# Kernel optimization log

Hardware: AMD Instinct MI355X
Metric: run time of the kernel (lower is better)

The kernel has to match this reference:

```python
import jax, jax.numpy as jnp
from jax import lax
import numpy as np

K_TOP = 100
NMS_THRESH = 0.5
SUBJECT_CATEGORY_ID = 0


def box_cxcywh_to_xyxy(b):
    cx, cy, w, h = b[..., 0], b[..., 1], b[..., 2], b[..., 3]
    return jnp.stack([cx - 0.5 * w, cy - 0.5 * h, cx + 0.5 * w, cy + 0.5 * h], axis=-1)


def _pairwise_iou(boxes):
    # boxes: [K,4] xyxy; uses the +1 pixel convention from the original numpy NMS
    x1, y1, x2, y2 = boxes[:, 0], boxes[:, 1], boxes[:, 2], boxes[:, 3]
    area = (x2 - x1 + 1.0) * (y2 - y1 + 1.0)
    xx1 = jnp.maximum(x1[:, None], x1[None, :])
    yy1 = jnp.maximum(y1[:, None], y1[None, :])
    xx2 = jnp.minimum(x2[:, None], x2[None, :])
    yy2 = jnp.minimum(y2[:, None], y2[None, :])
    w = jnp.maximum(0.0, xx2 - xx1 + 1.0)
    h = jnp.maximum(0.0, yy2 - yy1 + 1.0)
    inter = w * h
    union = area[:, None] + area[None, :] - inter
    return inter / union


def _nms_keep(sub_boxes, obj_boxes, obj_labels, hoi_scores):
    # Greedy grouped pairwise NMS for one image.
    # Grouping key degenerates to object label (subject cat and verb-row are constant).
    K = sub_boxes.shape[0]
    max_scores = hoi_scores.max(axis=-1)
    order = jnp.argsort(-max_scores)
    ovr = _pairwise_iou(sub_boxes) * _pairwise_iou(obj_boxes)  # [K,K]
    same_group = obj_labels[:, None] == obj_labels[None, :]
    ovr = jnp.where(same_group, ovr, 0.0)
    ovr_s = ovr[order][:, order]
    upper = jnp.triu(jnp.ones((K, K), dtype=bool), k=1)
    sup_mat = (ovr_s > NMS_THRESH) & upper  # suppression only of later (lower-score) items

    def body(i, st):
        suppressed, keep = st
        ki = jnp.logical_not(suppressed[i])
        keep = keep.at[i].set(ki)
        suppressed = suppressed | (ki & sup_mat[i])
        return suppressed, keep

    _, keep_sorted = lax.fori_loop(0, K, body, (jnp.zeros(K, bool), jnp.zeros(K, bool)))
    return jnp.zeros(K, bool).at[order].set(keep_sorted)


def setup_inputs() -> dict:
    key = jax.random.key(0)
    k1, k2, k3, k4, k5, k6 = jax.random.split(key, 6)
    B, Q, C, V = 256, 300, 81, 117
    return {
        "pred_obj_logits": jax.random.normal(k1, (B, Q, C), dtype=jnp.float32),
        "pred_verb_logits": jax.random.normal(k2, (B, Q, V), dtype=jnp.float32),
        "pred_sub_boxes": jax.random.uniform(k3, (B, Q, 4), dtype=jnp.float32),
        "pred_obj_boxes": jax.random.uniform(k4, (B, Q, 4), dtype=jnp.float32),
        "correct_mat": (jax.random.uniform(k5, (V, C), dtype=jnp.float32) > 0.3).astype(jnp.float32),
        "target_sizes": jax.random.randint(k6, (B, 2), 200, 640, dtype=jnp.int32),
    }


def reference(pred_obj_logits, pred_verb_logits, pred_sub_boxes, pred_obj_boxes, correct_mat, target_sizes):
    B, Q, C = pred_obj_logits.shape
    V = pred_verb_logits.shape[-1]

    obj_prob = jax.nn.softmax(pred_obj_logits, axis=-1)       # [B,Q,C]  (no_obj=False)
    verb_scores = jax.nn.sigmoid(pred_verb_logits)            # [B,Q,V]

    topk_values, topk_indexes = lax.top_k(obj_prob.reshape(B, Q * C), K_TOP)  # [B,100]
    topk_boxes = topk_indexes // C
    obj_labels = topk_indexes % C

    vs = jnp.take_along_axis(verb_scores, topk_boxes[..., None], axis=1)      # [B,100,V]
    ob = jnp.take_along_axis(pred_obj_boxes, topk_boxes[..., None], axis=1)   # [B,100,4]
    sb = jnp.take_along_axis(pred_sub_boxes, topk_boxes[..., None], axis=1)

    img_h = target_sizes[:, 0].astype(jnp.float32)
    img_w = target_sizes[:, 1].astype(jnp.float32)
    scale_fct = jnp.stack([img_w, img_h, img_w, img_h], axis=1)  # [B,4]
    sub_boxes = box_cxcywh_to_xyxy(sb) * scale_fct[:, None, :]
    obj_boxes = box_cxcywh_to_xyxy(ob) * scale_fct[:, None, :]

    hoi_scores = vs * topk_values[..., None]                    # [B,100,V]
    # masks[b,k,v] = correct_mat[v, obj_labels[b,k]]
    masks = correct_mat.T[obj_labels]                           # [B,100,V]
    hoi_scores = hoi_scores * masks

    keep = jax.vmap(_nms_keep)(sub_boxes, obj_boxes, obj_labels, hoi_scores)  # [B,100] bool
    final_scores = hoi_scores * keep[..., None].astype(hoi_scores.dtype)

    return final_scores, topk_values, obj_labels, sub_boxes, obj_boxes, keep
```

## Files before the change

kernel.cpp:

```cpp
#include <hip/hip_runtime.h>
#include <cmath>

#pragma clang fp contract(off)

#define NT 1024
constexpr int B_ = 256, Q_ = 300, C_ = 81, V_ = 117, K_ = 100;
constexpr int QC_ = Q_ * C_;
constexpr int KV_ = K_ * V_;
constexpr int NB  = 2048;
constexpr int CAP = 1024;

using u32 = unsigned int;
using u64 = unsigned long long;
using u16 = unsigned short;
using u8  = unsigned char;

#define PCUT 0.010f

constexpr int OFF_P16  = 0;
constexpr int OFF_HIST = 48600;
constexpr int OFF_RMAX = OFF_HIST + 8192;
constexpr int OFF_RINV = OFF_RMAX + 1200;
constexpr int OFF_BSUB = OFF_RINV + 1208;
constexpr int OFF_BOBJ = OFF_BSUB + 1600;
constexpr int OFF_SUPR = OFF_BOBJ + 1600;
constexpr int OFF_SELV = OFF_SUPR + 1600;
constexpr int OFF_SELI = OFF_SELV + 400;
constexpr int OFF_MAXB = OFF_SELI + 400;
constexpr int OFF_ORD  = OFF_MAXB + 400;
constexpr int OFF_LAB  = OFF_ORD + 104;
constexpr int OFF_MISC = OFF_LAB + 104;
constexpr int SMEM_SZ  = OFF_MISC + 48;
static_assert(SMEM_SZ <= 65536, "LDS overflow");
static_assert((OFF_BSUB & 15) == 0 && (OFF_BOBJ & 15) == 0, "b128 align");

__device__ __forceinline__ u64 shfl_xor_u64(u64 v, int mask) {
    u32 lo = (u32)v, hi = (u32)(v >> 32);
    lo = (u32)__shfl_xor((int)lo, mask, 64);
    hi = (u32)__shfl_xor((int)hi, mask, 64);
    return ((u64)hi << 32) | lo;
}

template <int CTRL>
__device__ __forceinline__ int dpp_i(int x) {
    return __builtin_amdgcn_update_dpp(0, x, CTRL, 0xF, 0xF, true);
}
__device__ __forceinline__ float bfly16(float x){ return __int_as_float(__builtin_amdgcn_ds_swizzle(__float_as_int(x), 0x401F)); }
__device__ __forceinline__ float bfly8 (float x){ return __int_as_float(dpp_i<0x128>(__float_as_int(x))); }
__device__ __forceinline__ float bfly4 (float x){ return __int_as_float(__builtin_amdgcn_ds_swizzle(__float_as_int(x), 0x101F)); }
__device__ __forceinline__ float bfly2 (float x){ return __int_as_float(dpp_i<0x4E>(__float_as_int(x))); }
__device__ __forceinline__ float bfly1 (float x){ return __int_as_float(dpp_i<0xB1>(__float_as_int(x))); }
__device__ __forceinline__ int ibfly4(int x){ return __builtin_amdgcn_ds_swizzle(x, 0x101F); }
__device__ __forceinline__ int ibfly2(int x){ return dpp_i<0x4E>(x); }
__device__ __forceinline__ int ibfly1(int x){ return dpp_i<0xB1>(x); }

__device__ __forceinline__ float iou4(float4 a, float4 b, float areaSum) {
    float xx1 = fmaxf(a.x, b.x);
    float yy1 = fmaxf(a.y, b.y);
    float xx2 = fminf(a.z, b.z);
    float yy2 = fminf(a.w, b.w);
    float w = fmaxf(0.f, xx2 - xx1 + 1.f);
    float h = fmaxf(0.f, yy2 - yy1 + 1.f);
    float inter = w * h;
    return inter / (areaSum - inter);
}

__global__ __launch_bounds__(NT, 4) void hoi_kernel(
    const float* __restrict__ obj_logits,
    const float* __restrict__ verb_logits,
    const float* __restrict__ sub_boxes_in,
    const float* __restrict__ obj_boxes_in,
    const float* __restrict__ cm,
    const int*   __restrict__ tsizes,
    float* __restrict__ out)
{
    const int b = blockIdx.x;
    const int tid = threadIdx.x;

    __shared__ __align__(16) u8 smem[SMEM_SZ];
    u16*   p16     = (u16*)(smem + OFF_P16);
    float* hs      = (float*)(smem + OFF_P16);
    u32*   hist    = (u32*)(smem + OFF_HIST);
    u64*   cand    = (u64*)(smem + OFF_HIST);
    float* asub    = (float*)(smem + OFF_HIST);
    float* aobj    = (float*)(smem + OFF_HIST + 512);
    float* rowmax  = (float*)(smem + OFF_RMAX);
    float* rinv    = (float*)(smem + OFF_RINV);
    float (*bsub)[4]   = (float(*)[4])(smem + OFF_BSUB);
    float (*bobj)[4]   = (float(*)[4])(smem + OFF_BOBJ);
    u32   (*supcol)[4] = (u32(*)[4])(smem + OFF_SUPR);
    float* sel_val = (float*)(smem + OFF_SELV);
    u32*   sel_idx = (u32*)(smem + OFF_SELI);
    u32*   maxbits = (u32*)(smem + OFF_MAXB);
    u8*    order8  = (u8*)(smem + OFF_ORD);
    u8*    lab8    = (u8*)(smem + OFF_LAB);
    u32*   skeep     = (u32*)(smem + OFF_MISC);
    u32*   keep_bits = (u32*)(smem + OFF_MISC + 16);
    u32*   s_cnt     = (u32*)(smem + OFF_MISC + 32);
    int*   sT        = (int*)(smem + OFF_MISC + 36);
    int*   sW        = (int*)(smem + OFF_MISC + 40);
    u32*   sAcc      = (u32*)(smem + OFF_MISC + 44);
    u32*   swsum   = (u32*)(smem + OFF_BSUB);
    u64*   wred    = (u64*)(smem + OFF_BOBJ);
    u64*   s_prev  = (u64*)(smem + OFF_SUPR);

    const float* lg = obj_logits + (size_t)b * QC_;

    for (int i = tid; i < NB; i += NT) hist[i] = 0;
    if (tid == 0) *s_cnt = 0;
    __syncthreads();

    {
        const int g = tid >> 5, l = tid & 31;
        const bool have2 = (l < C_ - 64);
        float v0[10], v1[10], v2[10];
        #pragma unroll
        for (int s = 0; s < 10; ++s) {
            int r = g + 32 * s;
            const float* row = lg + (size_t)((r < Q_ ? r : Q_ - 1) * C_);
            v0[s] = row[l];
            v1[s] = row[l + 32];
            v2[s] = have2 ? row[l + 64] : -INFINITY;
        }
        float m[10];
        #pragma unroll
        for (int s = 0; s < 10; ++s) m[s] = fmaxf(fmaxf(v0[s], v1[s]), v2[s]);
        #pragma unroll
        for (int s = 0; s < 10; ++s) m[s] = fmaxf(m[s], bfly16(m[s]));
        #pragma unroll
        for (int s = 0; s < 10; ++s) m[s] = fmaxf(m[s], bfly8(m[s]));
        #pragma unroll
        for (int s = 0; s < 10; ++s) m[s] = fmaxf(m[s], bfly4(m[s]));
        #pragma unroll
        for (int s = 0; s < 10; ++s) m[s] = fmaxf(m[s], bfly2(m[s]));
        #pragma unroll
        for (int s = 0; s < 10; ++s) m[s] = fmaxf(m[s], bfly1(m[s]));
        float e0[10], e1[10], e2[10], sm[10];
        #pragma unroll
        for (int s = 0; s < 10; ++s) {
            e0[s] = expf(v0[s] - m[s]);
            e1[s] = expf(v1[s] - m[s]);
            e2[s] = have2 ? expf(v2[s] - m[s]) : 0.f;
            sm[s] = e0[s] + e1[s] + e2[s];
        }
        #pragma unroll
        for (int s = 0; s < 10; ++s) sm[s] += bfly16(sm[s]);
        #pragma unroll
        for (int s = 0; s < 10; ++s) sm[s] += bfly8(sm[s]);
        #pragma unroll
        for (int s = 0; s < 10; ++s) sm[s] += bfly4(sm[s]);
        #pragma unroll
        for (int s = 0; s < 10; ++s) sm[s] += bfly2(sm[s]);
        #pragma unroll
        for (int s = 0; s < 10; ++s) sm[s] += bfly1(sm[s]);
        #pragma unroll
        for (int s = 0; s < 10; ++s) {
            int r = g + 32 * s;
            if (r < Q_) {
                float ri = 1.f / sm[s];
                float p0 = e0[s] * ri, p1 = e1[s] * ri;
                u32 x0 = __float_as_uint(p0), x1 = __float_as_uint(p1);
                p16[r * C_ + l]      = (u16)(x0 >> 16);
                p16[r * C_ + l + 32] = (u16)(x1 >> 16);
                if (p0 >= PCUT) atomicAdd(&hist[x0 >> 21], 1u);
                if (p1 >= PCUT) atomicAdd(&hist[x1 >> 21], 1u);
                if (have2) {
                    float p2 = e2[s] * ri;
                    u32 x2 = __float_as_uint(p2);
                    p16[r * C_ + l + 64] = (u16)(x2 >> 16);
                    if (p2 >= PCUT) atomicAdd(&hist[x2 >> 21], 1u);
                }
                if (l == 0) { rowmax[r] = m[s]; rinv[r] = ri; }
            }
        }
    }
    __syncthreads();

    u32 my_c, my_suf;
    {
        int t = tid;
        my_c = hist[2 * t] + hist[2 * t + 1];
        my_suf = my_c;
        #pragma unroll
        for (int off = 1; off < 64; off <<= 1) {
            u32 o = (u32)__shfl_down((int)my_suf, off, 64);
            my_suf += ((tid & 63) + off < 64) ? o : 0;
        }
        if ((tid & 63) == 0) swsum[tid >> 6] = my_suf;
    }
    __syncthreads();
    if (tid < 16) {
        u32 sufW = swsum[tid];
        #pragma unroll
        for (int off = 1; off < 16; off <<= 1) {
            u32 o = (u32)__shfl_down((int)sufW, off, 64);
            sufW += (tid + off < 16) ? o : 0;
        }
        u32 nxt = (u32)__shfl_down((int)sufW, 1, 64);
        if (tid == 15) nxt = 0;
        if (sufW >= (u32)K_ && nxt < (u32)K_) { *sW = tid; *sAcc = nxt; }
    }
    __syncthreads();
    if ((tid >> 6) == *sW) {
        u32 above = *sAcc + (my_suf - my_c);
        if (above < (u32)K_ && above + my_c >= (u32)K_) {
            u32 acc = above + hist[2 * tid + 1];
            *sT = (acc >= (u32)K_) ? (2 * tid + 1) : (2 * tid);
        }
    }
    __syncthreads();
    const int T = *sT;
    __syncthreads();

    for (int i0 = tid * 2; i0 < QC_; i0 += 2 * NT) {
        u32 two = *(const u32*)(p16 + i0);
        u32 pb0 = two & 0xFFFFu, pb1 = two >> 16;
        if ((int)(pb0 >> 5) >= T) {
            u32 pos = atomicAdd(s_cnt, 1u);
            if (pos < (u32)CAP) {
                int i = i0;
                int q = i / C_;
                float p = expf(lg[i] - rowmax[q]) * rinv[q];
                cand[pos] = ((u64)__float_as_uint(p) << 32) | (u32)(~i);
            }
        }
        if ((int)(pb1 >> 5) >= T) {
            u32 pos = atomicAdd(s_cnt, 1u);
            if (pos < (u32)CAP) {
                int i = i0 + 1;
                int q = i / C_;
                float p = expf(lg[i] - rowmax[q]) * rinv[q];
                cand[pos] = ((u64)__float_as_uint(p) << 32) | (u32)(~i);
            }
        }
    }
    __syncthreads();
    const int ncand = (int)*s_cnt;

    auto cswap = [](u64& a, u64& bb, bool up) {
        if ((a > bb) == up) { u64 t = a; a = bb; bb = t; }
    };

    if (ncand <= 256) {
        if (tid < 64) {
            u64 v0 = (tid < ncand) ? cand[tid] : 0ull;
            u64 v1 = (64 + tid < ncand) ? cand[64 + tid] : 0ull;
            u64 v2 = (128 + tid < ncand) ? cand[128 + tid] : 0ull;
            u64 v3 = (192 + tid < ncand) ? cand[192 + tid] : 0ull;
            for (int k = 2; k <= 256; k <<= 1) {
                for (int j = k >> 1; j > 0; j >>= 1) {
                    if (j == 128) {
                        cswap(v0, v2, true);
                        cswap(v1, v3, true);
                    } else if (j == 64) {
                        cswap(v0, v1, true);
                        cswap(v2, v3, (k == 256));
                    } else {
                        auto step = [&](u64& v, int ebase) {
                            u64 pv = shfl_xor_u64(v, j);
                            int e = ebase + tid;
                            bool up = ((e & k) == 0);
                            bool lower = ((e & j) == 0);
                            u64 mn = v < pv ? v : pv;
                            u64 mx = v < pv ? pv : v;
                            v = (lower == up) ? mn : mx;
                        };
                        step(v0, 0); step(v1, 64); step(v2, 128); step(v3, 192);
                    }
                }
            }
            int e2 = 128 + tid;
            if (e2 >= 156) {
                int t = 255 - e2;
                sel_val[t] = __uint_as_float((u32)(v2 >> 32));
                sel_idx[t] = ~(u32)v2;
            }
            int t3 = 255 - (192 + tid);
            sel_val[t3] = __uint_as_float((u32)(v3 >> 32));
            sel_idx[t3] = ~(u32)v3;
        }
    } else if (ncand <= CAP) {
        for (int e = tid; e < CAP; e += NT)
            if (e >= ncand) cand[e] = 0;
        __syncthreads();
        for (int k = 2; k <= CAP; k <<= 1) {
            for (int j = k >> 1; j > 0; j >>= 1) {
                int e = tid, partner = e ^ j;
                if (partner > e) {
                    u64 a = cand[e], bb = cand[partner];
                    bool up = ((e & k) == 0);
                    if ((a > bb) == up) { cand[e] = bb; cand[partner] = a; }
                }
                __syncthreads();
            }
        }
        if (tid < K_) {
            u64 m = cand[CAP - 1 - tid];
            sel_val[tid] = __uint_as_float((u32)(m >> 32));
            sel_idx[tid] = ~(u32)m;
        }
    } else {
        if (tid == 0) *s_prev = ~0ull;
        __syncthreads();
        for (int r = 0; r < K_; r++) {
            u64 prev = *s_prev;
            u64 local = 0;
            for (int i = tid; i < QC_; i += NT) {
                int q = i / C_;
                float p = expf(lg[i] - rowmax[q]) * rinv[q];
                u64 key = ((u64)__float_as_uint(p) << 32) | (u32)(~i);
                if (key < prev && key > local) local = key;
            }
            for (int off = 32; off > 0; off >>= 1) {
                u64 o = shfl_xor_u64(local, off);
                if (o > local) local = o;
            }
            if ((tid & 63) == 0) wred[tid >> 6] = local;
            __syncthreads();
            if (tid == 0) {
                u64 m = wred[0];
                for (int wv = 1; wv < 16; wv++) if (wred[wv] > m) m = wred[wv];
                *s_prev = m;
                u32 idx = ~(u32)m;
                if (idx >= (u32)QC_) idx = 0;
                sel_val[r] = __uint_as_float((u32)(m >> 32));
                sel_idx[r] = idx;
            }
            __syncthreads();
        }
    }
    __syncthreads();

    if (tid < 800) {
        int c = tid >> 3, j = tid & 7;
        u32 idx = sel_idx[c];
        int q = (int)idx / C_, lab = (int)idx - q * C_;
        const float* vrow = verb_logits + ((size_t)b * Q_ + q) * V_;
        float sv = sel_val[c];
        float xv[15], cv[15];
        #pragma unroll
        for (int k = 0; k < 15; ++k) {
            int v = j + 8 * k;
            int vc = v < V_ ? v : V_ - 1;
            xv[k] = vrow[vc];
            cv[k] = cm[vc * C_ + lab];
        }
        float m = 0.f;
        #pragma unroll
        for (int k = 0; k < 15; ++k) {
            int v = j + 8 * k;
            if (v < V_) {
                float hv = (1.f / (1.f + expf(-xv[k]))) * sv * cv[k];
                hs[c * V_ + v] = hv;
                m = fmaxf(m, hv);
            }
        }
        m = fmaxf(m, bfly4(m));
        m = fmaxf(m, bfly2(m));
        m = fmaxf(m, bfly1(m));
        if (j == 0) { maxbits[c] = __float_as_uint(m); lab8[c] = (u8)lab; }
    } else if (tid < 900) {
        int t = tid - 800;
        int idx = (int)sel_idx[t];
        int q = idx / C_;
        float iw = (float)tsizes[b * 2 + 1];
        float ih = (float)tsizes[b * 2 + 0];
        float4 sb = ((const float4*)sub_boxes_in)[(size_t)b * Q_ + q];
        float x1 = (sb.x - 0.5f * sb.z) * iw, y1 = (sb.y - 0.5f * sb.w) * ih;
        float x2 = (sb.x + 0.5f * sb.z) * iw, y2 = (sb.y + 0.5f * sb.w) * ih;
        bsub[t][0] = x1; bsub[t][1] = y1; bsub[t][2] = x2; bsub[t][3] = y2;
        asub[t] = (x2 - x1 + 1.f) * (y2 - y1 + 1.f);
        supcol[t][0] = 0; supcol[t][1] = 0; supcol[t][2] = 0; supcol[t][3] = 0;
    } else if (tid < 1000) {
        int t = tid - 900;
        int idx = (int)sel_idx[t];
        int q = idx / C_;
        float iw = (float)tsizes[b * 2 + 1];
        float ih = (float)tsizes[b * 2 + 0];
        float4 ob = ((const float4*)obj_boxes_in)[(size_t)b * Q_ + q];
        float x1 = (ob.x - 0.5f * ob.z) * iw, y1 = (ob.y - 0.5f * ob.w) * ih;
        float x2 = (ob.x + 0.5f * ob.z) * iw, y2 = (ob.y + 0.5f * ob.w) * ih;
        bobj[t][0] = x1; bobj[t][1] = y1; bobj[t][2] = x2; bobj[t][3] = y2;
        aobj[t] = (x2 - x1 + 1.f) * (y2 - y1 + 1.f);
    } else if (tid < 1004) {
        keep_bits[tid - 1000] = 0;
    }
    __syncthreads();

    if (tid < 800) {
        int r = tid >> 3, j = tid & 7;
        u64 kr = ((u64)maxbits[r] << 32) | (u32)(~r);
        int rank = 0;
        for (int k = 0; k < 13; k++) {
            int jj = j * 13 + k;
            if (jj < K_) {
                u64 kj = ((u64)maxbits[jj] << 32) | (u32)(~jj);
                rank += (kj > kr) ? 1 : 0;
            }
        }
        rank += ibfly4(rank);
        rank += ibfly2(rank);
        rank += ibfly1(rank);
        if (j == 0) order8[rank] = (u8)r;
    }
    __syncthreads();

    float* o0 = out;
    float* o1 = out + (size_t)B_ * KV_;
    float* o2 = o1 + (size_t)B_ * K_;
    float* o3 = o2 + (size_t)B_ * K_;
    float* o4 = o3 + (size_t)B_ * K_ * 4;
    float* o5 = o4 + (size_t)B_ * K_ * 4;

    if (tid < K_) {
        o1[(size_t)b * K_ + tid] = sel_val[tid];
        o2[(size_t)b * K_ + tid] = (float)(sel_idx[tid] % (u32)C_);
    }
    if (tid >= 128 && tid < 128 + K_ * 4) {
        int t = tid - 128;
        int r = t >> 2, k = t & 3;
        o3[((size_t)b * K_) * 4 + t] = bsub[r][k];
        o4[((size_t)b * K_) * 4 + t] = bobj[r][k];
    }

    for (int e = tid; e < K_ * K_; e += NT) {
        int i = e / K_, j = e - i * K_;
        if (j > i) {
            int ri = order8[i], rj = order8[j];
            u32 li = lab8[ri], lj = lab8[rj];
            if (li == lj) {
                float4 s_i = *(const float4*)bsub[ri];
                float4 s_j = *(const float4*)bsub[rj];
                float4 b_i = *(const float4*)bobj[ri];
                float4 b_j = *(const float4*)bobj[rj];
                float o = iou4(s_i, s_j, asub[ri] + asub[rj]) *
                          iou4(b_i, b_j, aobj[ri] + aobj[rj]);
                if (o > 0.5f)
                    atomicOr(&supcol[j][i >> 5], 1u << (i & 31));
            }
        }
    }
    __syncthreads();

    if (tid < 64) {
        u32 cA[4], cB[4];
        #pragma unroll
        for (int w = 0; w < 4; ++w) cA[w] = supcol[tid][w];
        #pragma unroll
        for (int w = 0; w < 4; ++w) cB[w] = (tid < K_ - 64) ? supcol[tid + 64][w] : 0u;
        bool sA = false, sB = false;
        u32 km[4] = {0, 0, 0, 0};
        #pragma unroll
        for (int i = 0; i < 64; ++i) {
            u64 bal = __ballot(sA);
            if (!((bal >> i) & 1)) {
                km[i >> 5] |= 1u << (i & 31);
                sA = sA || ((cA[i >> 5] >> (i & 31)) & 1u);
                sB = sB || ((cB[i >> 5] >> (i & 31)) & 1u);
            }
        }
        #pragma unroll
        for (int i = 64; i < K_; ++i) {
            u64 bal = __ballot(sB);
            if (!((bal >> (i - 64)) & 1)) {
                km[i >> 5] |= 1u << (i & 31);
                sA = sA || ((cA[i >> 5] >> (i & 31)) & 1u);
                sB = sB || ((cB[i >> 5] >> (i & 31)) & 1u);
            }
        }
        if (tid == 0) { skeep[0] = km[0]; skeep[1] = km[1]; skeep[2] = km[2]; skeep[3] = km[3]; }
    }
    __syncthreads();
    if (tid < K_) {
        if ((skeep[tid >> 5] >> (tid & 31)) & 1u) {
            int r = order8[tid];
            atomicOr(&keep_bits[r >> 5], 1u << (r & 31));
        }
    }
    __syncthreads();

    constexpr int KV4_ = KV_ / 4;
    for (int f4 = tid; f4 < KV4_; f4 += NT) {
        int base = f4 * 4;
        float4 h = *(const float4*)(hs + base);
        int r0 = base / V_, m0 = base - r0 * V_;
        int r1 = r0 + ((m0 + 1) >= V_ ? 1 : 0);
        int r2 = r0 + ((m0 + 2) >= V_ ? 1 : 0);
        int r3 = r0 + ((m0 + 3) >= V_ ? 1 : 0);
        float4 o;
        o.x = ((keep_bits[r0 >> 5] >> (r0 & 31)) & 1u) ? h.x : 0.f;
        o.y = ((keep_bits[r1 >> 5] >> (r1 & 31)) & 1u) ? h.y : 0.f;
        o.z = ((keep_bits[r2 >> 5] >> (r2 & 31)) & 1u) ? h.z : 0.f;
        o.w = ((keep_bits[r3 >> 5] >> (r3 & 31)) & 1u) ? h.w : 0.f;
        *(float4*)(o0 + (size_t)b * KV_ + base) = o;
    }
    if (tid < K_) {
        bool kp = (keep_bits[tid >> 5] >> (tid & 31)) & 1u;
        o5[(size_t)b * K_ + tid] = kp ? 1.f : 0.f;
    }
}

extern "C" void kernel_launch(void* const* d_in, const int* in_sizes, int n_in,
                              void* d_out, int out_size, void* d_ws, size_t ws_size,
                              hipStream_t stream) {
    const float* obj_logits  = (const float*)d_in[0];
    const float* verb_logits = (const float*)d_in[1];
    const float* sub_boxes   = (const float*)d_in[2];
    const float* obj_boxes   = (const float*)d_in[3];
    const float* cm          = (const float*)d_in[4];
    const int*   ts          = (const int*)d_in[5];
    hipLaunchKernelGGL(hoi_kernel, dim3(B_), dim3(NT), 0, stream,
                       obj_logits, verb_logits, sub_boxes, obj_boxes, cm, ts,
                       (float*)d_out);
}
```

Measured before the change: 136.0 us.

## Keep softmax probabilities in registers and shrink top-k histogram to 64 bins

Softmax probabilities now stay in per-thread registers instead of being written to LDS as 16-bit values and then rescanned. Candidate gathering reuses those registers, which removes the LDS scan and the global logit reload plus expf recompute. The histogram shrinks to 64 bins based on a bit-pattern cutoff, so the threshold search becomes a single-wavefront suffix scan with fewer barriers. The cost is about 30 extra live registers per thread under a 1024-thread launch bound, which risks spills, and a coarser histogram that may let more candidates through.

```diff
diff --git a/kernel.cpp b/kernel.cpp
--- a/kernel.cpp
+++ b/kernel.cpp
@@ -7,7 +7,6 @@
 constexpr int B_ = 256, Q_ = 300, C_ = 81, V_ = 117, K_ = 100;
 constexpr int QC_ = Q_ * C_;
 constexpr int KV_ = K_ * V_;
-constexpr int NB  = 2048;
 constexpr int CAP = 1024;
 
 using u32 = unsigned int;
@@ -15,9 +14,11 @@
 using u16 = unsigned short;
 using u8  = unsigned char;
 
-#define PCUT 0.010f
-
-constexpr int OFF_P16  = 0;
+constexpr u32 PCUT_BITS = 0x3C000000u;
+constexpr int BIN0 = 480;
+constexpr int NB   = 64;
+
+constexpr int OFF_HS   = 0;
 constexpr int OFF_HIST = 48600;
 constexpr int OFF_RMAX = OFF_HIST + 8192;
 constexpr int OFF_RINV = OFF_RMAX + 1200;
@@ -78,8 +79,7 @@
     const int tid = threadIdx.x;
 
     __shared__ __align__(16) u8 smem[SMEM_SZ];
-    u16*   p16     = (u16*)(smem + OFF_P16);
-    float* hs      = (float*)(smem + OFF_P16);
+    float* hs      = (float*)(smem + OFF_HS);
     u32*   hist    = (u32*)(smem + OFF_HIST);
     u64*   cand    = (u64*)(smem + OFF_HIST);
     float* asub    = (float*)(smem + OFF_HIST);
@@ -98,21 +98,19 @@
     u32*   keep_bits = (u32*)(smem + OFF_MISC + 16);
     u32*   s_cnt     = (u32*)(smem + OFF_MISC + 32);
     int*   sT        = (int*)(smem + OFF_MISC + 36);
-    int*   sW        = (int*)(smem + OFF_MISC + 40);
-    u32*   sAcc      = (u32*)(smem + OFF_MISC + 44);
-    u32*   swsum   = (u32*)(smem + OFF_BSUB);
     u64*   wred    = (u64*)(smem + OFF_BOBJ);
     u64*   s_prev  = (u64*)(smem + OFF_SUPR);
 
     const float* lg = obj_logits + (size_t)b * QC_;
 
-    for (int i = tid; i < NB; i += NT) hist[i] = 0;
+    if (tid < NB) hist[tid] = 0;
     if (tid == 0) *s_cnt = 0;
     __syncthreads();
 
+    const int g = tid >> 5, l = tid & 31;
+    const bool have2 = (l < C_ - 64);
+    float p0r[10], p1r[10], p2r[10];
     {
-        const int g = tid >> 5, l = tid & 31;
-        const bool have2 = (l < C_ - 64);
         float v0[10], v1[10], v2[10];
         #pragma unroll
         for (int s = 0; s < 10; ++s) {
@@ -156,19 +154,17 @@
         #pragma unroll
         for (int s = 0; s < 10; ++s) {
             int r = g + 32 * s;
+            float ri = 1.f / sm[s];
+            float p0 = e0[s] * ri, p1 = e1[s] * ri;
+            float p2 = have2 ? e2[s] * ri : 0.f;
+            p0r[s] = p0; p1r[s] = p1; p2r[s] = p2;
             if (r < Q_) {
-                float ri = 1.f / sm[s];
-                float p0 = e0[s] * ri, p1 = e1[s] * ri;
                 u32 x0 = __float_as_uint(p0), x1 = __float_as_uint(p1);
-                p16[r * C_ + l]      = (u16)(x0 >> 16);
-                p16[r * C_ + l + 32] = (u16)(x1 >> 16);
-                if (p0 >= PCUT) atomicAdd(&hist[x0 >> 21], 1u);
-                if (p1 >= PCUT) atomicAdd(&hist[x1 >> 21], 1u);
+                if (x0 >= PCUT_BITS) atomicAdd(&hist[(x0 >> 21) - BIN0], 1u);
+                if (x1 >= PCUT_BITS) atomicAdd(&hist[(x1 >> 21) - BIN0], 1u);
                 if (have2) {
-                    float p2 = e2[s] * ri;
                     u32 x2 = __float_as_uint(p2);
-                    p16[r * C_ + l + 64] = (u16)(x2 >> 16);
-                    if (p2 >= PCUT) atomicAdd(&hist[x2 >> 21], 1u);
+                    if (x2 >= PCUT_BITS) atomicAdd(&hist[(x2 >> 21) - BIN0], 1u);
                 }
                 if (l == 0) { rowmax[r] = m[s]; rinv[r] = ri; }
             }
@@ -176,61 +172,43 @@
     }
     __syncthreads();
 
-    u32 my_c, my_suf;
-    {
-        int t = tid;
-        my_c = hist[2 * t] + hist[2 * t + 1];
-        my_suf = my_c;
+    if (tid < 64) {
+        u32 suf = hist[tid];
         #pragma unroll
         for (int off = 1; off < 64; off <<= 1) {
-            u32 o = (u32)__shfl_down((int)my_suf, off, 64);
-            my_suf += ((tid & 63) + off < 64) ? o : 0;
-        }
-        if ((tid & 63) == 0) swsum[tid >> 6] = my_suf;
-    }
-    __syncthreads();
-    if (tid < 16) {
-        u32 sufW = swsum[tid];
-        #pragma unroll
-        for (int off = 1; off < 16; off <<= 1) {
-            u32 o = (u32)__shfl_down((int)sufW, off, 64);
-            sufW += (tid + off < 16) ? o : 0;
-        }
-        u32 nxt = (u32)__shfl_down((int)sufW, 1, 64);
-        if (tid == 15) nxt = 0;
-        if (sufW >= (u32)K_ && nxt < (u32)K_) { *sW = tid; *sAcc = nxt; }
-    }
-    __syncthreads();
-    if ((tid >> 6) == *sW) {
-        u32 above = *sAcc + (my_suf - my_c);
-        if (above < (u32)K_ && above + my_c >= (u32)K_) {
-            u32 acc = above + hist[2 * tid + 1];
-            *sT = (acc >= (u32)K_) ? (2 * tid + 1) : (2 * tid);
-        }
+            u32 o = (u32)__shfl_down((int)suf, off, 64);
+            suf += (tid + off < 64) ? o : 0;
+        }
+        u32 nxt = (u32)__shfl_down((int)suf, 1, 64);
+        if (tid == 63) nxt = 0;
+        if (suf >= (u32)K_ && nxt < (u32)K_) *sT = BIN0 + tid;
     }
     __syncthreads();
     const int T = *sT;
-    __syncthreads();
-
-    for (int i0 = tid * 2; i0 < QC_; i0 += 2 * NT) {
-        u32 two = *(const u32*)(p16 + i0);
-        u32 pb0 = two & 0xFFFFu, pb1 = two >> 16;
-        if ((int)(pb0 >> 5) >= T) {
-            u32 pos = atomicAdd(s_cnt, 1u);
-            if (pos < (u32)CAP) {
-                int i = i0;
-                int q = i / C_;
-                float p = expf(lg[i] - rowmax[q]) * rinv[q];
-                cand[pos] = ((u64)__float_as_uint(p) << 32) | (u32)(~i);
-            }
-        }
-        if ((int)(pb1 >> 5) >= T) {
-            u32 pos = atomicAdd(s_cnt, 1u);
-            if (pos < (u32)CAP) {
-                int i = i0 + 1;
-                int q = i / C_;
-                float p = expf(lg[i] - rowmax[q]) * rinv[q];
-                cand[pos] = ((u64)__float_as_uint(p) << 32) | (u32)(~i);
+
+    #pragma unroll
+    for (int s = 0; s < 10; ++s) {
+        int r = g + 32 * s;
+        if (r < Q_) {
+            u32 x0 = __float_as_uint(p0r[s]);
+            if ((int)(x0 >> 21) >= T) {
+                u32 pos = atomicAdd(s_cnt, 1u);
+                if (pos < (u32)CAP)
+                    cand[pos] = ((u64)x0 << 32) | (u32)(~(r * C_ + l));
+            }
+            u32 x1 = __float_as_uint(p1r[s]);
+            if ((int)(x1 >> 21) >= T) {
+                u32 pos = atomicAdd(s_cnt, 1u);
+                if (pos < (u32)CAP)
+                    cand[pos] = ((u64)x1 << 32) | (u32)(~(r * C_ + l + 32));
+            }
+            if (have2) {
+                u32 x2 = __float_as_uint(p2r[s]);
+                if ((int)(x2 >> 21) >= T) {
+                    u32 pos = atomicAdd(s_cnt, 1u);
+                    if (pos < (u32)CAP)
+                        cand[pos] = ((u64)x2 << 32) | (u32)(~(r * C_ + l + 64));
+                }
             }
         }
     }
```

Result: faster. 132.3 us (-2.8%).
